# Optimization experiments

Measured on AMD Instinct MI355X. Metric: run time of the kernel, lower is better.

Reference implementation:

```python
import jax, jax.numpy as jnp
import numpy as np
import math

N, C_IN, C_OUT, C_INT, S, T, V = 128, 64, 128, 32, 3, 64, 25
EPS = 1e-5

def make_pe(channel, joint_num, time_len, domain):
    if domain == 'spatial':
        pos = np.tile(np.arange(joint_num), time_len)  # j varies fastest
    else:
        pos = np.repeat(np.arange(time_len), joint_num)
    pos = pos[:, None].astype(np.float32)
    div = np.exp(np.arange(0, channel, 2).astype(np.float32) * (-math.log(10000.0) / channel))
    pe = np.zeros((time_len * joint_num, channel), dtype=np.float32)
    pe[:, 0::2] = np.sin(pos * div)
    pe[:, 1::2] = np.cos(pos * div)
    pe = pe.reshape(time_len, joint_num, channel).transpose(2, 0, 1)[None]  # [1,C,T,V]
    return jnp.asarray(pe)

def _conv1x1(x, w, b):
    # x: [N,Ci,T,V], w: [Co,Ci] -> [N,Co,T,V]
    return jnp.einsum('nctv,oc->notv', x, w) + b[None, :, None, None]

def _bn(x, p):
    g, b, m, v = p  # p: [4,C] = (gamma, beta, running_mean, running_var), eval-mode BN
    scale = (g / jnp.sqrt(v + EPS))[None, :, None, None]
    return (x - m[None, :, None, None]) * scale + b[None, :, None, None]

def _lrelu(x):
    return jnp.where(x >= 0, x, 0.1 * x)


def setup_inputs() -> dict:
    key = jax.random.key(0)
    ks = iter(jax.random.split(key, 48))
    def w(shape, fan):
        return jax.random.normal(next(ks), shape, jnp.float32) / np.float32(np.sqrt(fan))
    def bias(c):
        return 0.01 * jax.random.normal(next(ks), (c,), jnp.float32)
    def bn(c):
        k1, k2, k3, k4 = jax.random.split(next(ks), 4)
        return jnp.stack([
            1.0 + 0.1 * jax.random.normal(k1, (c,), jnp.float32),
            0.1 * jax.random.normal(k2, (c,), jnp.float32),
            0.1 * jax.random.normal(k3, (c,), jnp.float32),
            jax.random.uniform(k4, (c,), jnp.float32, minval=0.5, maxval=1.5),
        ])
    return dict(
        x=jax.random.normal(next(ks), (N, C_IN, T, V), jnp.float32),
        w_qk_s=w((2 * S * C_INT, C_IN), C_IN), b_qk_s=bias(2 * S * C_INT),
        alphas=jnp.ones((1, S, 1, 1), jnp.float32),
        att0s=jnp.ones((1, S, V, V), jnp.float32) / V + 0.01 * jax.random.normal(next(ks), (1, S, V, V), jnp.float32),
        w_outs=w((C_OUT, S * C_IN), S * C_IN), b_outs=bias(C_OUT), bn_outs=bn(C_OUT),
        w_ffs=w((C_OUT, C_OUT), C_OUT), b_ffs=bias(C_OUT), bn_ffs=bn(C_OUT),
        w_ds1=w((C_OUT, C_IN), C_IN), b_ds1=bias(C_OUT), bn_ds1=bn(C_OUT),
        w_ds2=w((C_OUT, C_IN), C_IN), b_ds2=bias(C_OUT), bn_ds2=bn(C_OUT),
        w_qk_t=w((2 * S * C_INT, C_OUT), C_OUT), b_qk_t=bias(2 * S * C_INT),
        alphat=jnp.ones((1, S, 1, 1), jnp.float32),
        att0t=jnp.eye(T, dtype=jnp.float32)[None, None] + 0.01 * jax.random.normal(next(ks), (1, S, T, T), jnp.float32),
        w_outt=w((C_OUT, S * C_OUT), S * C_OUT), b_outt=bias(C_OUT), bn_outt=bn(C_OUT),
        w_fft=w((C_OUT, C_OUT), C_OUT), b_fft=bias(C_OUT), bn_fft=bn(C_OUT),
        w_dt1=w((C_OUT, C_OUT), C_OUT), b_dt1=bias(C_OUT), bn_dt1=bn(C_OUT),
        w_dt2=w((C_OUT, C_OUT), C_OUT), b_dt2=bias(C_OUT), bn_dt2=bn(C_OUT),
    )


def reference(x, w_qk_s, b_qk_s, alphas, att0s, w_outs, b_outs, bn_outs,
              w_ffs, b_ffs, bn_ffs, w_ds1, b_ds1, bn_ds1, w_ds2, b_ds2, bn_ds2,
              w_qk_t, b_qk_t, alphat, att0t, w_outt, b_outt, bn_outt,
              w_fft, b_fft, bn_fft, w_dt1, b_dt1, bn_dt1, w_dt2, b_dt2, bn_dt2):
    n = x.shape[0]
    pe_s = make_pe(C_IN, V, T, 'spatial')
    pe_t = make_pe(C_OUT, V, T, 'temporal')

    # ---- spatial attention ----
    y = x + pe_s
    qk = _conv1x1(y, w_qk_s, b_qk_s).reshape(n, 2 * S, C_INT, T, V)
    q, k = qk[:, :S], qk[:, S:]
    att = jnp.tanh(jnp.einsum('nsctu,nsctv->nsuv', q, k) / (C_INT * T)) * alphas + att0s
    # dropout p=0 -> identity
    y = jnp.einsum('nctu,nsuv->nsctv', x, att).reshape(n, S * C_IN, T, V)
    y = _bn(_conv1x1(y, w_outs, b_outs), bn_outs)
    y = _lrelu(_bn(_conv1x1(x, w_ds1, b_ds1), bn_ds1) + y)
    y2 = _bn(_conv1x1(y, w_ffs, b_ffs), bn_ffs)
    y = _lrelu(_bn(_conv1x1(x, w_ds2, b_ds2), bn_ds2) + y2)

    # ---- temporal attention ----
    z = y + pe_t
    qk = _conv1x1(z, w_qk_t, b_qk_t).reshape(n, 2 * S, C_INT, T, V)
    q, k = qk[:, :S], qk[:, S:]
    att = jnp.tanh(jnp.einsum('nsctv,nscqv->nstq', q, k) / (C_INT * V)) * alphat + att0t
    z = jnp.einsum('nctv,nstq->nscqv', y, att).reshape(n, S * C_OUT, T, V)
    z = _bn(_conv1x1(z, w_outt, b_outt), bn_outt)
    z = _lrelu(_bn(_conv1x1(y, w_dt1, b_dt1), bn_dt1) + z)
    z2 = _bn(_conv1x1(z, w_fft, b_fft), bn_fft)
    z = _lrelu(_bn(_conv1x1(y, w_dt2, b_dt2), bn_dt2) + z2)
    return z
```

## Files before the change

### kernel.cpp

```cpp
#include <hip/hip_runtime.h>
#include <math.h>

#define N_    128
#define CIN   64
#define COUT  128
#define CINT  32
#define S_    3
#define T_    64
#define V_    25
#define EPSF  1e-5f
#define LN1E4 9.210340371976184f
#define P_    (N_*T_*V_)

typedef __attribute__((ext_vector_type(8))) short bf16x8;
typedef __attribute__((ext_vector_type(4))) unsigned short bf16x4;
typedef __attribute__((ext_vector_type(4))) float f32x4;

#define MFMA(a,b,c) __builtin_amdgcn_mfma_f32_16x16x32_bf16(a,b,c,0,0,0)

#define OFF_WQS    0u
#define OFF_WQT    24576u
#define OFF_WOUTS  73728u
#define OFF_WDS1   122880u
#define OFF_WFFS   139264u
#define OFF_WDS2   172032u
#define OFF_WOUTT  188416u
#define OFF_WDT1   286720u
#define OFF_WFFT   319488u
#define OFF_WDT2   352256u
#define OFF_WOV    385024u
#define OFF_WOT    409600u
#define OFF_SHA    434176u
#define OFF_SHB    434688u
#define OFF_SHC    435200u
#define OFF_SHD    435712u
#define OFF_OV     436224u
#define OFF_OT     641024u
#define OFF_ATTST  845824u
#define OFF_ATTTT  1632256u
#define OFF_XCL    4777984u
#define OFF_YCL    30992384u
#define OFF_RB     83421184u
#define OFF_RA     135849984u

__device__ __forceinline__ unsigned short f2bf(float f) {
  union { float f; unsigned int u; } v; v.f = f;
  unsigned int u = v.u;
  return (unsigned short)((u + 0x7FFFu + ((u >> 16) & 1u)) >> 16);
}
__device__ __forceinline__ float bnscale(const float* bn, int o) {
  return bn[o] * rsqrtf(bn[3*COUT + o] + EPSF);
}
__device__ __forceinline__ float bnshift(const float* bn, const float* b, int o) {
  return (b[o] - bn[2*COUT + o]) * bnscale(bn, o) + bn[COUT + o];
}
__device__ __forceinline__ float pe_val(int c, int p, float inv) {
  float freq = expf(-(float)(c >> 1) * inv);
  float arg = (float)p * freq;
  return (c & 1) ? cosf(arg) : sinf(arg);
}

__global__ __launch_bounds__(256) void k_prep(
    const float* __restrict__ wqks, const float* __restrict__ bqks,
    const float* __restrict__ wouts, const float* __restrict__ bouts, const float* __restrict__ bnouts,
    const float* __restrict__ wffs, const float* __restrict__ bffs, const float* __restrict__ bnffs,
    const float* __restrict__ wds1, const float* __restrict__ bds1, const float* __restrict__ bnds1,
    const float* __restrict__ wds2, const float* __restrict__ bds2, const float* __restrict__ bnds2,
    const float* __restrict__ wqkt, const float* __restrict__ bqkt,
    const float* __restrict__ woutt, const float* __restrict__ boutt, const float* __restrict__ bnoutt,
    const float* __restrict__ wfft, const float* __restrict__ bfft, const float* __restrict__ bnfft,
    const float* __restrict__ wdt1, const float* __restrict__ bdt1, const float* __restrict__ bndt1,
    const float* __restrict__ wdt2, const float* __restrict__ bdt2, const float* __restrict__ bndt2,
    char* __restrict__ ws)
{
  int i = blockIdx.x * 256 + threadIdx.x;
  unsigned short* WQS   = (unsigned short*)(ws + OFF_WQS);
  unsigned short* WQT   = (unsigned short*)(ws + OFF_WQT);
  unsigned short* WOUTS = (unsigned short*)(ws + OFF_WOUTS);
  unsigned short* WDS1  = (unsigned short*)(ws + OFF_WDS1);
  unsigned short* WFFS  = (unsigned short*)(ws + OFF_WFFS);
  unsigned short* WDS2  = (unsigned short*)(ws + OFF_WDS2);
  unsigned short* WOUTT = (unsigned short*)(ws + OFF_WOUTT);
  unsigned short* WDT1  = (unsigned short*)(ws + OFF_WDT1);
  unsigned short* WFFT  = (unsigned short*)(ws + OFF_WFFT);
  unsigned short* WDT2  = (unsigned short*)(ws + OFF_WDT2);
  unsigned short* WOV   = (unsigned short*)(ws + OFF_WOV);
  unsigned short* WOT   = (unsigned short*)(ws + OFF_WOT);
  float* SHA = (float*)(ws + OFF_SHA);
  float* SHB = (float*)(ws + OFF_SHB);
  float* SHC = (float*)(ws + OFF_SHC);
  float* SHD = (float*)(ws + OFF_SHD);
  unsigned short* OV = (unsigned short*)(ws + OFF_OV);
  unsigned short* OT = (unsigned short*)(ws + OFF_OT);

  if (i < 12288) { WQS[i] = f2bf(wqks[i]); }
  else if (i < 36864) { int j = i - 12288; WQT[j] = f2bf(wqkt[j]); }
  else if (i < 61440) { int j = i - 36864; int o = j / 192; WOUTS[j] = f2bf(wouts[j] * bnscale(bnouts, o)); }
  else if (i < 69632) { int j = i - 61440; int o = j / 64;  WDS1[j]  = f2bf(wds1[j]  * bnscale(bnds1, o)); }
  else if (i < 86016) { int j = i - 69632; int o = j / 128; WFFS[j]  = f2bf(wffs[j]  * bnscale(bnffs, o)); }
  else if (i < 94208) { int j = i - 86016; int o = j / 64;  WDS2[j]  = f2bf(wds2[j]  * bnscale(bnds2, o)); }
  else if (i < 143360){ int j = i - 94208; int o = j / 384; WOUTT[j] = f2bf(woutt[j] * bnscale(bnoutt, o)); }
  else if (i < 159744){ int j = i - 143360; int o = j / 128; WDT1[j] = f2bf(wdt1[j] * bnscale(bndt1, o)); }
  else if (i < 176128){ int j = i - 159744; int o = j / 128; WFFT[j] = f2bf(wfft[j] * bnscale(bnfft, o)); }
  else if (i < 192512){ int j = i - 176128; int o = j / 128; WDT2[j] = f2bf(wdt2[j] * bnscale(bndt2, o)); }
  else if (i < 204800){
    int j = i - 192512; int o = j >> 6, u = j & 63;
    float acc = 0.f;
    if (u < V_) {
      acc = bqks[o];
      const float inv = 2.0f * LN1E4 / (float)CIN;
      for (int c = 0; c < CIN; ++c) acc += wqks[o*CIN + c] * pe_val(c, u, inv);
    }
    WOV[j] = f2bf(acc);
  }
  else if (i < 217088){
    int j = i - 204800; int o = j >> 6, t = j & 63;
    float acc = bqkt[o];
    const float inv = 2.0f * LN1E4 / (float)COUT;
    for (int c = 0; c < COUT; ++c) acc += wqkt[o*COUT + c] * pe_val(c, t, inv);
    WOT[j] = f2bf(acc);
  }
  else if (i < 217600){
    int j = i - 217088; int o = j & 127; int g = j >> 7;
    if (g == 0) SHA[o] = bnshift(bnouts, bouts, o) + bnshift(bnds1, bds1, o);
    if (g == 1) SHB[o] = bnshift(bnffs, bffs, o)   + bnshift(bnds2, bds2, o);
    if (g == 2) SHC[o] = bnshift(bnoutt, boutt, o) + bnshift(bndt1, bdt1, o);
    if (g == 3) SHD[o] = bnshift(bnfft, bfft, o)   + bnshift(bndt2, bdt2, o);
  }
  else if (i < 320000){
    int j = i - 217600; int rem = j >> 6, u = j & 63;
    OV[j] = (u == rem % 25) ? (unsigned short)0x3F80 : (unsigned short)0;
  }
  else if (i < 422400){
    int j = i - 320000; int rem = j >> 6, u = j & 63;
    OT[j] = (u == rem / 25) ? (unsigned short)0x3F80 : (unsigned short)0;
  }
}

__global__ __launch_bounds__(256) void k_convert(const float* __restrict__ x,
                                                 unsigned short* __restrict__ xcl)
{
  __shared__ float xs[64][26];
  int b = blockIdx.x; int n = b >> 6, t = b & 63; int tid = threadIdx.x;
  for (int i = tid; i < 1600; i += 256) {
    int c = i / 25, v = i % 25;
    xs[c][v] = x[(((size_t)(n*64 + c))*64 + t)*25 + v];
  }
  __syncthreads();
  size_t clbase = ((size_t)(n*64 + t)) * 1600;
  for (int i = tid; i < 1600; i += 256) { int v = i >> 6, c = i & 63; xcl[clbase + i] = f2bf(xs[c][v]); }
}

template<int K1, int K2, int NOSUB, int NOFULL, int HASSHIFT, int LRELU, int OMODE, int A2MOD>
__global__ __launch_bounds__(256, 2) void k_conv(
    const unsigned short* __restrict__ A1, const unsigned short* __restrict__ A2,
    const unsigned short* __restrict__ W1, const unsigned short* __restrict__ W2,
    const float* __restrict__ shift, void* __restrict__ outp)
{
  constexpr int K   = K1 + K2;
  constexpr int NK  = K / 32;
  constexpr int NK1 = K1 / 32;
  constexpr int GR  = K / 8;
  __shared__ __align__(16) unsigned short Wl[NOSUB * K];

  const int oy = blockIdx.y;
  for (int i = threadIdx.x; i < NOSUB * GR; i += 256) {
    int o = i / GR, c = i % GR;
    int og = oy * NOSUB + o;
    int k = c * 8;
    const unsigned short* src = (k < K1) ? (W1 + (size_t)og * K1 + k)
                                         : (W2 + (size_t)og * K2 + (k - K1));
    int cs = c ^ (o & 7);
    *(int4*)&Wl[o * K + cs * 8] = *(const int4*)src;
  }

  const int lane = threadIdx.x & 63;
  const int wave = threadIdx.x >> 6;
  const int col  = lane & 15;
  const int quad = lane >> 4;
  const int pos0 = blockIdx.x * 256 + wave * 64;

  bf16x8 a[4][NK];
  const int remw = pos0 % 1600;
#pragma unroll
  for (int m = 0; m < 4; ++m) {
    const int pos = pos0 + m * 16 + col;
#pragma unroll
    for (int ks = 0; ks < NK; ++ks) {
      const unsigned short* p;
      if (ks < NK1) {
        p = A1 + (size_t)pos * K1 + ks * 32;
      } else {
        int row = pos;
        if (A2MOD) { int r2 = remw + m * 16 + col; if (r2 >= 1600) r2 -= 1600; row = r2; }
        p = A2 + (size_t)row * K2 + (ks - NK1) * 32;
      }
      a[m][ks] = *(const bf16x8*)(p + quad * 8);
    }
  }

  int sb[4];
#pragma unroll
  for (int m = 0; m < 4; ++m) {
    int pm = pos0 + m * 16 + quad * 4;
    if (OMODE == 0) sb[m] = pm * NOFULL + oy * NOSUB + col;
    else { int n = pm / 1600, rm = pm % 1600; sb[m] = n * 204800 + rm; }
  }

  __syncthreads();

  for (int ot = 0; ot < NOSUB / 16; ++ot) {
    const int orow = ot * 16 + col;
    f32x4 acc[4];
#pragma unroll
    for (int m = 0; m < 4; ++m) acc[m] = (f32x4){0.f, 0.f, 0.f, 0.f};
#pragma unroll
    for (int ks = 0; ks < NK; ++ks) {
      int cs = (ks * 4 + quad) ^ (col & 7);
      bf16x8 w = *(const bf16x8*)&Wl[orow * K + cs * 8];
#pragma unroll
      for (int m = 0; m < 4; ++m) acc[m] = MFMA(a[m][ks], w, acc[m]);
    }
    float sh = 0.f;
    if (HASSHIFT) sh = shift[oy * NOSUB + orow];
    if (OMODE == 2) {
      float* of = (float*)outp;
#pragma unroll
      for (int m = 0; m < 4; ++m) {
        float4 o4;
        float v0 = acc[m][0] + sh, v1 = acc[m][1] + sh, v2 = acc[m][2] + sh, v3 = acc[m][3] + sh;
        if (LRELU) {
          v0 = v0 >= 0.f ? v0 : 0.1f * v0; v1 = v1 >= 0.f ? v1 : 0.1f * v1;
          v2 = v2 >= 0.f ? v2 : 0.1f * v2; v3 = v3 >= 0.f ? v3 : 0.1f * v3;
        }
        o4.x = v0; o4.y = v1; o4.z = v2; o4.w = v3;
        *(float4*)&of[(size_t)sb[m] + (size_t)orow * 1600] = o4;
      }
    } else {
      unsigned short* oc = (unsigned short*)outp;
#pragma unroll
      for (int m = 0; m < 4; ++m)
#pragma unroll
        for (int r = 0; r < 4; ++r) {
          float val = acc[m][r] + sh;
          if (LRELU) val = val >= 0.f ? val : 0.1f * val;
          oc[(size_t)(sb[m] + r * NOFULL) + ot * 16] = f2bf(val);
        }
    }
  }
}

__global__ __launch_bounds__(64) void k_att_s(const unsigned short* __restrict__ qks,
                                              const float* __restrict__ alphas,
                                              const float* __restrict__ att0s,
                                              unsigned short* __restrict__ attsT)
{
  int b = blockIdx.x; int n = b / 3, s = b % 3;
  int lane = threadIdx.x; int col = lane & 15, quad = lane >> 4;
  f32x4 acc[2][2];
#pragma unroll
  for (int a = 0; a < 2; ++a)
#pragma unroll
    for (int c = 0; c < 2; ++c) acc[a][c] = (f32x4){0.f, 0.f, 0.f, 0.f};

  for (int t = 0; t < 64; ++t) {
    size_t rowb = ((size_t)(n * 64 + t)) * 25;
    bf16x8 afr[2], bfr[2];
#pragma unroll
    for (int ut = 0; ut < 2; ++ut)
      afr[ut] = *(const bf16x8*)(qks + (rowb + ut * 16 + col) * 192 + s * 32 + quad * 8);
#pragma unroll
    for (int vt = 0; vt < 2; ++vt)
      bfr[vt] = *(const bf16x8*)(qks + (rowb + vt * 16 + col) * 192 + 96 + s * 32 + quad * 8);
#pragma unroll
    for (int ut = 0; ut < 2; ++ut)
#pragma unroll
      for (int vt = 0; vt < 2; ++vt)
        acc[ut][vt] = MFMA(afr[ut], bfr[vt], acc[ut][vt]);
  }
  float alpha = alphas[s];
#pragma unroll
  for (int ut = 0; ut < 2; ++ut)
#pragma unroll
    for (int vt = 0; vt < 2; ++vt)
#pragma unroll
      for (int r = 0; r < 4; ++r) {
        int u = ut * 16 + quad * 4 + r;
        int v = vt * 16 + col;
        if (v < V_) {
          float val = 0.f;
          if (u < V_)
            val = tanhf(acc[ut][vt][r] * (1.0f / 2048.0f)) * alpha + att0s[(s * 25 + u) * 25 + v];
          attsT[((size_t)((n * 3 + s) * 32) + v) * 32 + u] = f2bf(val);
        }
      }
}

__global__ __launch_bounds__(64) void k_einsum_s(const float* __restrict__ x,
                                                 const unsigned short* __restrict__ attsT,
                                                 unsigned short* __restrict__ ys)
{
  int b = blockIdx.x; int n = b >> 6, t = b & 63;
  int lane = threadIdx.x; int col = lane & 15, quad = lane >> 4;
  bf16x8 bfr[4];
#pragma unroll
  for (int ct = 0; ct < 4; ++ct) {
    const float* p = x + ((size_t)(n * 64 + ct * 16 + col) * 64 + t) * 25;
    bf16x8 f;
#pragma unroll
    for (int j = 0; j < 8; ++j) {
      int u = quad * 8 + j;
      f[j] = (u < V_) ? (short)f2bf(p[u]) : (short)0;
    }
    bfr[ct] = f;
  }
  size_t posbase = ((size_t)(n * 64 + t)) * 25;
#pragma unroll
  for (int s = 0; s < 3; ++s) {
    bf16x8 afr[2];
#pragma unroll
    for (int vt = 0; vt < 2; ++vt)
      afr[vt] = *(const bf16x8*)(attsT + ((size_t)((n * 3 + s) * 32) + vt * 16 + col) * 32 + quad * 8);
#pragma unroll
    for (int vt = 0; vt < 2; ++vt)
#pragma unroll
      for (int ct = 0; ct < 4; ++ct) {
        f32x4 acc = {0.f, 0.f, 0.f, 0.f};
        acc = MFMA(afr[vt], bfr[ct], acc);
#pragma unroll
        for (int r = 0; r < 4; ++r) {
          int v = vt * 16 + quad * 4 + r;
          if (v < V_)
            ys[(posbase + v) * 192 + s * 64 + ct * 16 + col] = f2bf(acc[r]);
        }
      }
  }
}

__global__ __launch_bounds__(256) void k_att_t(const unsigned short* __restrict__ qkt,
                                               const float* __restrict__ alphat,
                                               const float* __restrict__ att0t,
                                               unsigned short* __restrict__ atttT)
{
  int b = blockIdx.x; int n = b / 3, s = b % 3;
  int wave = threadIdx.x >> 6; int lane = threadIdx.x & 63;
  int col = lane & 15, quad = lane >> 4;
  int mt = wave;
  f32x4 acc[4];
#pragma unroll
  for (int q = 0; q < 4; ++q) acc[q] = (f32x4){0.f, 0.f, 0.f, 0.f};

  for (int v = 0; v < V_; ++v) {
    bf16x8 a = *(const bf16x8*)(qkt + (((size_t)(n * 64 + mt * 16 + col)) * 25 + v) * 192 + s * 32 + quad * 8);
#pragma unroll
    for (int nt = 0; nt < 4; ++nt) {
      bf16x8 bb = *(const bf16x8*)(qkt + (((size_t)(n * 64 + nt * 16 + col)) * 25 + v) * 192 + 96 + s * 32 + quad * 8);
      acc[nt] = MFMA(a, bb, acc[nt]);
    }
  }
  float alpha = alphat[s];
#pragma unroll
  for (int nt = 0; nt < 4; ++nt)
#pragma unroll
    for (int r = 0; r < 4; ++r) {
      int ti = mt * 16 + quad * 4 + r;
      int q  = nt * 16 + col;
      float val = tanhf(acc[nt][r] * (1.0f / 800.0f)) * alpha + att0t[(s * 64 + ti) * 64 + q];
      atttT[((size_t)((n * 3 + s) * 64) + q) * 64 + ti] = f2bf(val);
    }
}

__global__ __launch_bounds__(256) void k_fused(
    const unsigned short* __restrict__ ycl,
    const unsigned short* __restrict__ atttT,
    const unsigned short* __restrict__ Woutt, const unsigned short* __restrict__ Wdt1,
    const float* __restrict__ shiftC, unsigned short* __restrict__ z1)
{
  __shared__ unsigned short z[64 * 392];
  __shared__ unsigned short yT[128 * 72];
  int b = blockIdx.x; int n = b / 25, v = b % 25;
  int wave = threadIdx.x >> 6; int lane = threadIdx.x & 63;
  int col = lane & 15, quad = lane >> 4;
  int tid = threadIdx.x;

  for (int i = tid; i < 128 * 64; i += 256) {
    int t = i >> 7, c = i & 127;
    yT[c * 72 + t] = ycl[(((size_t)(n * 64 + t)) * 25 + v) * 128 + c];
  }
  __syncthreads();

  bf16x8 ya[2][2];
#pragma unroll
  for (int ci = 0; ci < 2; ++ci) {
    int ctg = wave * 2 + ci;
    ya[ci][0] = *(const bf16x8*)&yT[(ctg * 16 + col) * 72 + quad * 8];
    ya[ci][1] = *(const bf16x8*)&yT[(ctg * 16 + col) * 72 + 32 + quad * 8];
  }
#pragma unroll
  for (int s = 0; s < 3; ++s) {
#pragma unroll
    for (int ci = 0; ci < 2; ++ci) {
      int ctg = wave * 2 + ci;
#pragma unroll
      for (int qt = 0; qt < 4; ++qt) {
        const unsigned short* bp = atttT + ((size_t)((n * 3 + s) * 64) + qt * 16 + col) * 64 + quad * 8;
        f32x4 acc = {0.f, 0.f, 0.f, 0.f};
        acc = MFMA(ya[ci][0], *(const bf16x8*)bp, acc);
        acc = MFMA(ya[ci][1], *(const bf16x8*)(bp + 32), acc);
        bf16x4 pk;
        pk[0] = f2bf(acc[0]); pk[1] = f2bf(acc[1]); pk[2] = f2bf(acc[2]); pk[3] = f2bf(acc[3]);
        *(bf16x4*)&z[(qt * 16 + col) * 392 + s * 128 + ctg * 16 + quad * 4] = pk;
      }
    }
  }
  __syncthreads();

  f32x4 acc[2][4];
#pragma unroll
  for (int a = 0; a < 2; ++a)
#pragma unroll
    for (int q = 0; q < 4; ++q) acc[a][q] = (f32x4){0.f, 0.f, 0.f, 0.f};

  for (int ks = 0; ks < 12; ++ks) {
    bf16x8 afr[4];
#pragma unroll
    for (int qt = 0; qt < 4; ++qt)
      afr[qt] = *(const bf16x8*)&z[(qt * 16 + col) * 392 + ks * 32 + quad * 8];
#pragma unroll
    for (int oi = 0; oi < 2; ++oi) {
      int otg = wave * 2 + oi;
      bf16x8 bb = *(const bf16x8*)(Woutt + (size_t)(otg * 16 + col) * 384 + ks * 32 + quad * 8);
#pragma unroll
      for (int qt = 0; qt < 4; ++qt) acc[oi][qt] = MFMA(afr[qt], bb, acc[oi][qt]);
    }
  }
  for (int ks = 0; ks < 4; ++ks) {
    bf16x8 afr[4];
#pragma unroll
    for (int qt = 0; qt < 4; ++qt)
      afr[qt] = *(const bf16x8*)(ycl + (((size_t)(n * 64 + qt * 16 + col)) * 25 + v) * 128 + ks * 32 + quad * 8);
#pragma unroll
    for (int oi = 0; oi < 2; ++oi) {
      int otg = wave * 2 + oi;
      bf16x8 bb = *(const bf16x8*)(Wdt1 + (size_t)(otg * 16 + col) * 128 + ks * 32 + quad * 8);
#pragma unroll
      for (int qt = 0; qt < 4; ++qt) acc[oi][qt] = MFMA(afr[qt], bb, acc[oi][qt]);
    }
  }
#pragma unroll
  for (int oi = 0; oi < 2; ++oi) {
    int o = (wave * 2 + oi) * 16 + col;
    float sh = shiftC[o];
#pragma unroll
    for (int qt = 0; qt < 4; ++qt)
#pragma unroll
      for (int r = 0; r < 4; ++r) {
        int q = qt * 16 + quad * 4 + r;
        float val = acc[oi][qt][r] + sh;
        val = (val >= 0.f) ? val : 0.1f * val;
        z1[(((size_t)(n * 64 + q)) * 25 + v) * 128 + o] = f2bf(val);
      }
  }
}

extern "C" void kernel_launch(void* const* d_in, const int* in_sizes, int n_in,
                              void* d_out, int out_size, void* d_ws, size_t ws_size,
                              hipStream_t stream)
{
  const float* x       = (const float*)d_in[0];
  const float* w_qk_s  = (const float*)d_in[1];
  const float* b_qk_s  = (const float*)d_in[2];
  const float* alphas  = (const float*)d_in[3];
  const float* att0s   = (const float*)d_in[4];
  const float* w_outs  = (const float*)d_in[5];
  const float* b_outs  = (const float*)d_in[6];
  const float* bn_outs = (const float*)d_in[7];
  const float* w_ffs   = (const float*)d_in[8];
  const float* b_ffs   = (const float*)d_in[9];
  const float* bn_ffs  = (const float*)d_in[10];
  const float* w_ds1   = (const float*)d_in[11];
  const float* b_ds1   = (const float*)d_in[12];
  const float* bn_ds1  = (const float*)d_in[13];
  const float* w_ds2   = (const float*)d_in[14];
  const float* b_ds2   = (const float*)d_in[15];
  const float* bn_ds2  = (const float*)d_in[16];
  const float* w_qk_t  = (const float*)d_in[17];
  const float* b_qk_t  = (const float*)d_in[18];
  const float* alphat  = (const float*)d_in[19];
  const float* att0t   = (const float*)d_in[20];
  const float* w_outt  = (const float*)d_in[21];
  const float* b_outt  = (const float*)d_in[22];
  const float* bn_outt = (const float*)d_in[23];
  const float* w_fft   = (const float*)d_in[24];
  const float* b_fft   = (const float*)d_in[25];
  const float* bn_fft  = (const float*)d_in[26];
  const float* w_dt1   = (const float*)d_in[27];
  const float* b_dt1   = (const float*)d_in[28];
  const float* bn_dt1  = (const float*)d_in[29];
  const float* w_dt2   = (const float*)d_in[30];
  const float* b_dt2   = (const float*)d_in[31];
  const float* bn_dt2  = (const float*)d_in[32];

  char* ws = (char*)d_ws;
  unsigned short* WQS   = (unsigned short*)(ws + OFF_WQS);
  unsigned short* WQT   = (unsigned short*)(ws + OFF_WQT);
  unsigned short* WOUTS = (unsigned short*)(ws + OFF_WOUTS);
  unsigned short* WDS1  = (unsigned short*)(ws + OFF_WDS1);
  unsigned short* WFFS  = (unsigned short*)(ws + OFF_WFFS);
  unsigned short* WDS2  = (unsigned short*)(ws + OFF_WDS2);
  unsigned short* WOUTT = (unsigned short*)(ws + OFF_WOUTT);
  unsigned short* WDT1  = (unsigned short*)(ws + OFF_WDT1);
  unsigned short* WFFT  = (unsigned short*)(ws + OFF_WFFT);
  unsigned short* WDT2  = (unsigned short*)(ws + OFF_WDT2);
  unsigned short* WOV   = (unsigned short*)(ws + OFF_WOV);
  unsigned short* WOT   = (unsigned short*)(ws + OFF_WOT);
  float* SHA = (float*)(ws + OFF_SHA);
  float* SHB = (float*)(ws + OFF_SHB);
  float* SHC = (float*)(ws + OFF_SHC);
  float* SHD = (float*)(ws + OFF_SHD);
  unsigned short* OV    = (unsigned short*)(ws + OFF_OV);
  unsigned short* OT    = (unsigned short*)(ws + OFF_OT);
  unsigned short* ATTST = (unsigned short*)(ws + OFF_ATTST);
  unsigned short* ATTTT = (unsigned short*)(ws + OFF_ATTTT);
  unsigned short* XCL   = (unsigned short*)(ws + OFF_XCL);
  unsigned short* YCL   = (unsigned short*)(ws + OFF_YCL);
  unsigned short* RB    = (unsigned short*)(ws + OFF_RB);
  unsigned short* RA    = (unsigned short*)(ws + OFF_RA);

  k_prep<<<1650, 256, 0, stream>>>(
      w_qk_s, b_qk_s, w_outs, b_outs, bn_outs, w_ffs, b_ffs, bn_ffs,
      w_ds1, b_ds1, bn_ds1, w_ds2, b_ds2, bn_ds2, w_qk_t, b_qk_t,
      w_outt, b_outt, bn_outt, w_fft, b_fft, bn_fft,
      w_dt1, b_dt1, bn_dt1, w_dt2, b_dt2, bn_dt2, ws);

  k_convert<<<N_ * T_, 256, 0, stream>>>(x, XCL);

  k_conv<64, 64, 192, 192, 0, 0, 0, 1><<<dim3(P_ / 256, 1), 256, 0, stream>>>(
      XCL, OV, WQS, WOV, nullptr, RA);

  k_att_s<<<N_ * S_, 64, 0, stream>>>(RA, alphas, att0s, ATTST);
  k_einsum_s<<<N_ * T_, 64, 0, stream>>>(x, ATTST, RA);

  k_conv<192, 64, 128, 128, 1, 1, 0, 0><<<dim3(P_ / 256, 1), 256, 0, stream>>>(
      RA, XCL, WOUTS, WDS1, SHA, RB);

  k_conv<128, 64, 128, 128, 1, 1, 0, 0><<<dim3(P_ / 256, 1), 256, 0, stream>>>(
      RB, XCL, WFFS, WDS2, SHB, YCL);

  k_conv<128, 64, 96, 192, 0, 0, 0, 1><<<dim3(P_ / 256, 2), 256, 0, stream>>>(
      YCL, OT, WQT, WOT, nullptr, RA);

  k_att_t<<<N_ * S_, 256, 0, stream>>>(RA, alphat, att0t, ATTTT);

  k_fused<<<N_ * V_, 256, 0, stream>>>(YCL, ATTTT, WOUTT, WDT1, SHC, RB);

  k_conv<128, 128, 128, 128, 1, 1, 2, 0><<<dim3(P_ / 256, 1), 256, 0, stream>>>(
      RB, YCL, WFFT, WDT2, SHD, d_out);
}
```

Baseline: 744.8 us.

## Split spatial attention over waves, read bf16 x, swizzle fused LDS tile

k_att_s now runs with 256 threads, where each wave accumulates a quarter of the time steps and the partial sums are reduced through shared memory. This raises parallelism from 384 single-wave blocks. k_einsum_s reads the already converted channel-last bf16 XCL instead of fp32 x, which cuts load bytes and conversion work. k_fused drops its transposed yT staging buffer and loads y fragments directly from global memory, uses an XOR-swizzled unpadded z tile to avoid bank conflicts, and requests two blocks per CU. The direct strided global loads in k_fused may be less coalesced than the old staged transpose.

```diff
diff --git a/kernel.cpp b/kernel.cpp
--- a/kernel.cpp
+++ b/kernel.cpp
@@ -250,20 +250,24 @@
   }
 }
 
-__global__ __launch_bounds__(64) void k_att_s(const unsigned short* __restrict__ qks,
-                                              const float* __restrict__ alphas,
-                                              const float* __restrict__ att0s,
-                                              unsigned short* __restrict__ attsT)
-{
+__global__ __launch_bounds__(256) void k_att_s(const unsigned short* __restrict__ qks,
+                                               const float* __restrict__ alphas,
+                                               const float* __restrict__ att0s,
+                                               unsigned short* __restrict__ attsT)
+{
+  __shared__ float red[4][1024];
   int b = blockIdx.x; int n = b / 3, s = b % 3;
-  int lane = threadIdx.x; int col = lane & 15, quad = lane >> 4;
+  int tid = threadIdx.x;
+  int wave = tid >> 6, lane = tid & 63;
+  int col = lane & 15, quad = lane >> 4;
   f32x4 acc[2][2];
 #pragma unroll
   for (int a = 0; a < 2; ++a)
 #pragma unroll
     for (int c = 0; c < 2; ++c) acc[a][c] = (f32x4){0.f, 0.f, 0.f, 0.f};
 
-  for (int t = 0; t < 64; ++t) {
+  for (int tt = 0; tt < 16; ++tt) {
+    int t = wave * 16 + tt;
     size_t rowb = ((size_t)(n * 64 + t)) * 25;
     bf16x8 afr[2], bfr[2];
 #pragma unroll
@@ -278,25 +282,40 @@
       for (int vt = 0; vt < 2; ++vt)
         acc[ut][vt] = MFMA(afr[ut], bfr[vt], acc[ut][vt]);
   }
+#pragma unroll
+  for (int ut = 0; ut < 2; ++ut)
+#pragma unroll
+    for (int vt = 0; vt < 2; ++vt)
+#pragma unroll
+      for (int r = 0; r < 4; ++r)
+        red[wave][(ut * 8 + vt * 4 + r) * 64 + lane] = acc[ut][vt][r];
+  __syncthreads();
+
   float alpha = alphas[s];
-#pragma unroll
-  for (int ut = 0; ut < 2; ++ut)
-#pragma unroll
-    for (int vt = 0; vt < 2; ++vt)
-#pragma unroll
-      for (int r = 0; r < 4; ++r) {
-        int u = ut * 16 + quad * 4 + r;
-        int v = vt * 16 + col;
-        if (v < V_) {
-          float val = 0.f;
-          if (u < V_)
-            val = tanhf(acc[ut][vt][r] * (1.0f / 2048.0f)) * alpha + att0s[(s * 25 + u) * 25 + v];
-          attsT[((size_t)((n * 3 + s) * 32) + v) * 32 + u] = f2bf(val);
-        }
-      }
-}
-
-__global__ __launch_bounds__(64) void k_einsum_s(const float* __restrict__ x,
+  float4 r0 = *(const float4*)&red[0][tid * 4];
+  float4 r1 = *(const float4*)&red[1][tid * 4];
+  float4 r2 = *(const float4*)&red[2][tid * 4];
+  float4 r3 = *(const float4*)&red[3][tid * 4];
+  float sum4[4] = { r0.x + r1.x + r2.x + r3.x, r0.y + r1.y + r2.y + r3.y,
+                    r0.z + r1.z + r2.z + r3.z, r0.w + r1.w + r2.w + r3.w };
+#pragma unroll
+  for (int k = 0; k < 4; ++k) {
+    int slot = tid * 4 + k;
+    int lane_l = slot & 63;
+    int f = slot >> 6;
+    int ut = f >> 3, vt = (f >> 2) & 1, r = f & 3;
+    int u = ut * 16 + (lane_l >> 4) * 4 + r;
+    int v = vt * 16 + (lane_l & 15);
+    if (v < V_) {
+      float val = 0.f;
+      if (u < V_)
+        val = tanhf(sum4[k] * (1.0f / 2048.0f)) * alpha + att0s[(s * 25 + u) * 25 + v];
+      attsT[((size_t)((n * 3 + s) * 32) + v) * 32 + u] = f2bf(val);
+    }
+  }
+}
+
+__global__ __launch_bounds__(64) void k_einsum_s(const unsigned short* __restrict__ xcl,
                                                  const unsigned short* __restrict__ attsT,
                                                  unsigned short* __restrict__ ys)
 {
@@ -305,12 +324,12 @@
   bf16x8 bfr[4];
 #pragma unroll
   for (int ct = 0; ct < 4; ++ct) {
-    const float* p = x + ((size_t)(n * 64 + ct * 16 + col) * 64 + t) * 25;
+    const unsigned short* base = xcl + ((size_t)(n * 64 + t) * 25) * 64 + ct * 16 + col;
     bf16x8 f;
 #pragma unroll
     for (int j = 0; j < 8; ++j) {
       int u = quad * 8 + j;
-      f[j] = (u < V_) ? (short)f2bf(p[u]) : (short)0;
+      f[j] = (u < V_) ? (short)base[u * 64] : (short)0;
     }
     bfr[ct] = f;
   }
@@ -370,31 +389,31 @@
     }
 }
 
-__global__ __launch_bounds__(256) void k_fused(
+__global__ __launch_bounds__(256, 2) void k_fused(
     const unsigned short* __restrict__ ycl,
     const unsigned short* __restrict__ atttT,
     const unsigned short* __restrict__ Woutt, const unsigned short* __restrict__ Wdt1,
     const float* __restrict__ shiftC, unsigned short* __restrict__ z1)
 {
-  __shared__ unsigned short z[64 * 392];
-  __shared__ unsigned short yT[128 * 72];
+  __shared__ unsigned short z[64 * 384];
   int b = blockIdx.x; int n = b / 25, v = b % 25;
   int wave = threadIdx.x >> 6; int lane = threadIdx.x & 63;
   int col = lane & 15, quad = lane >> 4;
-  int tid = threadIdx.x;
-
-  for (int i = tid; i < 128 * 64; i += 256) {
-    int t = i >> 7, c = i & 127;
-    yT[c * 72 + t] = ycl[(((size_t)(n * 64 + t)) * 25 + v) * 128 + c];
-  }
-  __syncthreads();
 
   bf16x8 ya[2][2];
 #pragma unroll
   for (int ci = 0; ci < 2; ++ci) {
-    int ctg = wave * 2 + ci;
-    ya[ci][0] = *(const bf16x8*)&yT[(ctg * 16 + col) * 72 + quad * 8];
-    ya[ci][1] = *(const bf16x8*)&yT[(ctg * 16 + col) * 72 + 32 + quad * 8];
+    int c = (wave * 2 + ci) * 16 + col;
+#pragma unroll
+    for (int kk = 0; kk < 2; ++kk) {
+      bf16x8 f;
+#pragma unroll
+      for (int j = 0; j < 8; ++j) {
+        int t = kk * 32 + quad * 8 + j;
+        f[j] = (short)ycl[(((size_t)(n * 64 + t)) * 25 + v) * 128 + c];
+      }
+      ya[ci][kk] = f;
+    }
   }
 #pragma unroll
   for (int s = 0; s < 3; ++s) {
@@ -409,7 +428,11 @@
         acc = MFMA(ya[ci][1], *(const bf16x8*)(bp + 32), acc);
         bf16x4 pk;
         pk[0] = f2bf(acc[0]); pk[1] = f2bf(acc[1]); pk[2] = f2bf(acc[2]); pk[3] = f2bf(acc[3]);
-        *(bf16x4*)&z[(qt * 16 + col) * 392 + s * 128 + ctg * 16 + quad * 4] = pk;
+        int q  = qt * 16 + col;
+        int sc = s * 128 + ctg * 16 + quad * 4;
+        int g  = sc >> 3;
+        int ph = q * 384 + ((g & ~7) + ((g & 7) ^ (q & 7))) * 8 + (sc & 7);
+        *(bf16x4*)&z[ph] = pk;
       }
     }
   }
@@ -424,8 +447,12 @@
   for (int ks = 0; ks < 12; ++ks) {
     bf16x8 afr[4];
 #pragma unroll
-    for (int qt = 0; qt < 4; ++qt)
-      afr[qt] = *(const bf16x8*)&z[(qt * 16 + col) * 392 + ks * 32 + quad * 8];
+    for (int qt = 0; qt < 4; ++qt) {
+      int q = qt * 16 + col;
+      int g = ks * 4 + quad;
+      int ph = q * 384 + ((g & ~7) + ((g & 7) ^ (q & 7))) * 8;
+      afr[qt] = *(const bf16x8*)&z[ph];
+    }
 #pragma unroll
     for (int oi = 0; oi < 2; ++oi) {
       int otg = wave * 2 + oi;
@@ -538,8 +565,8 @@
   k_conv<64, 64, 192, 192, 0, 0, 0, 1><<<dim3(P_ / 256, 1), 256, 0, stream>>>(
       XCL, OV, WQS, WOV, nullptr, RA);
 
-  k_att_s<<<N_ * S_, 64, 0, stream>>>(RA, alphas, att0s, ATTST);
-  k_einsum_s<<<N_ * T_, 64, 0, stream>>>(x, ATTST, RA);
+  k_att_s<<<N_ * S_, 256, 0, stream>>>(RA, alphas, att0s, ATTST);
+  k_einsum_s<<<N_ * T_, 64, 0, stream>>>(XCL, ATTST, RA);
 
   k_conv<192, 64, 128, 128, 1, 1, 0, 0><<<dim3(P_ / 256, 1), 256, 0, stream>>>(
       RA, XCL, WOUTS, WDS1, SHA, RB);
```

New measurement: 673.8 us. 9.5% less time.
